# Kernel optimization log

Hardware: AMD Instinct MI355X
Metric: run time of the kernel (lower is better)

Reference implementation:

```python
import jax, jax.numpy as jnp
import numpy as np

B, S, D, H = 2, 2048, 1024, 16
HD = D // H  # head_dim = 64


def setup_inputs() -> dict:
    key = jax.random.key(0)
    ks = jax.random.split(key, 5)
    scale = 1.0 / np.sqrt(D)
    return {
        "x": jax.random.normal(ks[0], (B, S, D), dtype=jnp.float32),
        "w_qkv": jax.random.normal(ks[1], (D, 3 * D), dtype=jnp.float32) * scale,
        "b_qkv": jnp.zeros((3 * D,), dtype=jnp.float32),
        "w_out": jax.random.normal(ks[2], (D, D), dtype=jnp.float32) * scale,
        "b_out": jnp.zeros((D,), dtype=jnp.float32),
    }


def reference(x, w_qkv, b_qkv, w_out, b_out):
    b, s, d = x.shape
    qkv = x @ w_qkv + b_qkv  # [B,S,3D]
    q, k, v = jnp.split(qkv, 3, axis=-1)
    # [B,S,D] -> [B,H,S,HD]
    def to_heads(t):
        return t.reshape(b, s, H, HD).transpose(0, 2, 1, 3)
    q, k, v = to_heads(q), to_heads(k), to_heads(v)
    scores = jnp.einsum("bhqd,bhkd->bhqk", q, k) / np.sqrt(HD)
    attn = jax.nn.softmax(scores, axis=-1)
    out = jnp.einsum("bhqk,bhkd->bhqd", attn, v)  # [B,H,S,HD]
    out = out.transpose(0, 2, 1, 3).reshape(b, s, d)
    return out @ w_out + b_out
```

## Files before the change

### kernel.cpp

```cpp
#include <hip/hip_runtime.h>
#include <hip/hip_bf16.h>
#include <math.h>


typedef __bf16 bf16;
typedef __attribute__((ext_vector_type(8))) __bf16 bf16x8;
typedef __attribute__((ext_vector_type(4))) __bf16 bf16x4;
typedef __attribute__((ext_vector_type(4))) float f32x4;

#define B_ 2
#define S_ 2048
#define D_ 1024
#define H_ 16
#define HD_ 64

__device__ __forceinline__ f32x4 mfma16(bf16x8 a, bf16x8 b, f32x4 c) {
    return __builtin_amdgcn_mfma_f32_16x16x32_bf16(a, b, c, 0, 0, 0);
}

__device__ __forceinline__ void gload_lds16(const void* g, void* l) {
    __builtin_amdgcn_global_load_lds(
        (const __attribute__((address_space(1))) void*)g,
        (__attribute__((address_space(3))) void*)l, 16, 0, 0);
}


__global__ __launch_bounds__(256) void convert_x_kernel(
        const float* __restrict__ x, bf16* __restrict__ xb) {
    int i = blockIdx.x * 256 + threadIdx.x;
    float4 v = ((const float4*)x)[i];
    bf16x4 o = { (bf16)v.x, (bf16)v.y, (bf16)v.z, (bf16)v.w };
    ((bf16x4*)xb)[i] = o;
}

__global__ __launch_bounds__(256) void transpose_w_kernel(
        const float* __restrict__ src, bf16* __restrict__ dst, int K, int N) {
    int n0 = blockIdx.x * 64, k0 = blockIdx.y * 64;
    int lane = threadIdx.x & 63, wv = threadIdx.x >> 6;
    int k = k0 + lane;
    for (int i = 0; i < 16; i++) {
        int n = n0 + wv * 16 + i;
        dst[(size_t)n * K + k] = (bf16)src[(size_t)k * N + n];
    }
}

template <bool OUT_BF16>
__global__ __launch_bounds__(256) void gemm_bt_kernel(
        const bf16* __restrict__ A, const bf16* __restrict__ Bt,
        const float* __restrict__ bias, void* __restrict__ Cout,
        int M, int N, int K) {
    __shared__ bf16 As[128 * 32];
    __shared__ bf16 Bs[128 * 32];
    const int t = threadIdx.x;
    const int lane = t & 63, w = t >> 6;
    const int g = lane >> 4, c = lane & 15;
    const int m0 = blockIdx.y * 128, n0 = blockIdx.x * 128;
    const int wm = (w >> 1) * 64, wn = (w & 1) * 64;

    f32x4 acc[4][4];
    for (int i = 0; i < 4; i++)
        for (int j = 0; j < 4; j++) acc[i][j] = (f32x4){0.f, 0.f, 0.f, 0.f};

    const size_t rowB = (size_t)K * 2;
    const char* Abase = (const char*)A + (size_t)m0 * rowB;
    const char* Bbase = (const char*)Bt + (size_t)n0 * rowB;

    for (int kt = 0; kt < K; kt += 32) {
        for (int i = 0; i < 2; i++) {
            int boff = (w * 2 + i) * 1024 + lane * 16;
            int row = boff >> 6;
            int colb = boff & 63;
            gload_lds16(Abase + (size_t)row * rowB + (size_t)kt * 2 + colb,
                        (char*)As + (w * 2 + i) * 1024);
            gload_lds16(Bbase + (size_t)row * rowB + (size_t)kt * 2 + colb,
                        (char*)Bs + (w * 2 + i) * 1024);
        }
        __syncthreads();
        bf16x8 af[4], bfr[4];
        for (int mt = 0; mt < 4; mt++)
            af[mt] = *(const bf16x8*)&As[(wm + mt * 16 + c) * 32 + g * 8];
        for (int nt = 0; nt < 4; nt++)
            bfr[nt] = *(const bf16x8*)&Bs[(wn + nt * 16 + c) * 32 + g * 8];
        for (int mt = 0; mt < 4; mt++)
            for (int nt = 0; nt < 4; nt++)
                acc[mt][nt] = mfma16(af[mt], bfr[nt], acc[mt][nt]);
        __syncthreads();
    }

    for (int mt = 0; mt < 4; mt++) {
        for (int nt = 0; nt < 4; nt++) {
            int col = n0 + wn + nt * 16 + c;
            float bv = bias[col];
            for (int r = 0; r < 4; r++) {
                int row = m0 + wm + mt * 16 + g * 4 + r;
                float v = acc[mt][nt][r] + bv;
                if (OUT_BF16)
                    ((bf16*)Cout)[(size_t)row * N + col] = (bf16)v;
                else
                    ((float*)Cout)[(size_t)row * N + col] = v;
            }
        }
    }
}

#define KT_ 64
#define LPK_ 72
#define LPP_ 76

__global__ __launch_bounds__(256) void attn_kernel(
        const bf16* __restrict__ qkv, bf16* __restrict__ out) {
    __shared__ bf16 Ks[2][KT_ * LPK_];
    __shared__ bf16 Vs[2][HD_ * LPK_];
    __shared__ bf16 Ps[4][2][16 * LPP_];

    const int t = threadIdx.x;
    const int lane = t & 63, wv = t >> 6;
    const int g = lane >> 4, c = lane & 15;
    const int bh = blockIdx.y, b = bh >> 4, h = bh & 15;
    const int qbase = blockIdx.x * 128 + wv * 16;

    const float cs = 0.125f * 1.44269504088896341f;

    bf16x8 qf[2][2];
    for (int ch = 0; ch < 2; ch++) {
        const size_t qoff = (size_t)(b * S_ + qbase + ch * 64 + c) * (3 * D_) + h * HD_;
        qf[ch][0] = *(const bf16x8*)(qkv + qoff + g * 8);
        qf[ch][1] = *(const bf16x8*)(qkv + qoff + 32 + g * 8);
    }

    const bf16 one = (bf16)1.0f;
    const bf16x8 ones = { one, one, one, one, one, one, one, one };

    f32x4 o[2][4];
    for (int ch = 0; ch < 2; ch++)
        for (int i = 0; i < 4; i++) o[ch][i] = (f32x4){0.f, 0.f, 0.f, 0.f};
    f32x4 accl[2];
    accl[0] = accl[1] = (f32x4){0.f, 0.f, 0.f, 0.f};

    const int kk = t >> 2, kh = (t & 3) * 16;
    const int vk = t & 63, vh = (t >> 6) * 16;

    const bf16* kbase = qkv + (size_t)(b * S_) * (3 * D_) + D_ + h * HD_;
    const bf16* vbase = qkv + (size_t)(b * S_) * (3 * D_) + 2 * D_ + h * HD_;

    bf16x8 kr0, kr1, vr0, vr1;
    {
        const bf16* ks = kbase + (size_t)kk * (3 * D_) + kh;
        kr0 = *(const bf16x8*)ks;
        kr1 = *(const bf16x8*)(ks + 8);
        const bf16* vs = vbase + (size_t)vk * (3 * D_) + vh;
        vr0 = *(const bf16x8*)vs;
        vr1 = *(const bf16x8*)(vs + 8);
        *(bf16x8*)&Ks[0][kk * LPK_ + kh] = kr0;
        *(bf16x8*)&Ks[0][kk * LPK_ + kh + 8] = kr1;
        for (int j = 0; j < 8; j++) Vs[0][(vh + j) * LPK_ + vk] = vr0[j];
        for (int j = 0; j < 8; j++) Vs[0][(vh + 8 + j) * LPK_ + vk] = vr1[j];
    }
    __syncthreads();

    for (int tile = 0; tile < S_ / KT_; tile++) {
        const int buf = tile & 1;
        const bool has_next = (tile + 1) < (S_ / KT_);
        if (has_next) {
            const int j0 = (tile + 1) * KT_;
            const bf16* ks = kbase + (size_t)(j0 + kk) * (3 * D_) + kh;
            kr0 = *(const bf16x8*)ks;
            kr1 = *(const bf16x8*)(ks + 8);
            const bf16* vs = vbase + (size_t)(j0 + vk) * (3 * D_) + vh;
            vr0 = *(const bf16x8*)vs;
            vr1 = *(const bf16x8*)(vs + 8);
        }

        bf16x8 kf0[4], kf1[4];
        for (int kt = 0; kt < 4; kt++) {
            kf0[kt] = *(const bf16x8*)&Ks[buf][(kt * 16 + c) * LPK_ + g * 8];
            kf1[kt] = *(const bf16x8*)&Ks[buf][(kt * 16 + c) * LPK_ + 32 + g * 8];
        }

        f32x4 s[2][4];
        for (int ch = 0; ch < 2; ch++)
            for (int kt = 0; kt < 4; kt++) {
                f32x4 acc = (f32x4){0.f, 0.f, 0.f, 0.f};
                acc = mfma16(qf[ch][0], kf0[kt], acc);
                acc = mfma16(qf[ch][1], kf1[kt], acc);
                s[ch][kt] = acc;
            }

        for (int ch = 0; ch < 2; ch++) {
            bf16* P = Ps[wv][ch];
            for (int kt = 0; kt < 4; kt++)
                for (int r = 0; r < 4; r++)
                    P[(g * 4 + r) * LPP_ + kt * 16 + c] =
                        (bf16)__builtin_amdgcn_exp2f(s[ch][kt][r] * cs);
        }

        bf16x8 pf[2][2];
        for (int ch = 0; ch < 2; ch++) {
            pf[ch][0] = *(const bf16x8*)&Ps[wv][ch][c * LPP_ + g * 8];
            pf[ch][1] = *(const bf16x8*)&Ps[wv][ch][c * LPP_ + 32 + g * 8];
            accl[ch] = mfma16(pf[ch][0], ones, accl[ch]);
            accl[ch] = mfma16(pf[ch][1], ones, accl[ch]);
        }

        for (int nt = 0; nt < 4; nt++) {
            bf16x8 vf0 = *(const bf16x8*)&Vs[buf][(nt * 16 + c) * LPK_ + g * 8];
            bf16x8 vf1 = *(const bf16x8*)&Vs[buf][(nt * 16 + c) * LPK_ + 32 + g * 8];
            for (int ch = 0; ch < 2; ch++) {
                o[ch][nt] = mfma16(pf[ch][0], vf0, o[ch][nt]);
                o[ch][nt] = mfma16(pf[ch][1], vf1, o[ch][nt]);
            }
        }

        if (has_next) {
            *(bf16x8*)&Ks[buf ^ 1][kk * LPK_ + kh] = kr0;
            *(bf16x8*)&Ks[buf ^ 1][kk * LPK_ + kh + 8] = kr1;
            for (int j = 0; j < 8; j++) Vs[buf ^ 1][(vh + j) * LPK_ + vk] = vr0[j];
            for (int j = 0; j < 8; j++) Vs[buf ^ 1][(vh + 8 + j) * LPK_ + vk] = vr1[j];
        }
        __syncthreads();
    }

    for (int ch = 0; ch < 2; ch++)
        for (int r = 0; r < 4; r++) {
            float inv = 1.f / accl[ch][r];
            int row = qbase + ch * 64 + g * 4 + r;
            size_t base = (size_t)(b * S_ + row) * D_ + h * HD_;
            for (int nt = 0; nt < 4; nt++)
                out[base + nt * 16 + c] = (bf16)(o[ch][nt][r] * inv);
        }
}


extern "C" void kernel_launch(void* const* d_in, const int* in_sizes, int n_in,
                              void* d_out, int out_size, void* d_ws, size_t ws_size,
                              hipStream_t stream) {
    const float* x     = (const float*)d_in[0];
    const float* w_qkv = (const float*)d_in[1];
    const float* b_qkv = (const float*)d_in[2];
    const float* w_out = (const float*)d_in[3];
    const float* b_out = (const float*)d_in[4];
    float* out = (float*)d_out;

    char* ws = (char*)d_ws;
    bf16* x_bf    = (bf16*)(ws + 0);
    bf16* attn_bf = x_bf;
    bf16* wqkv_t  = (bf16*)(ws + (8u << 20));
    bf16* wout_t  = (bf16*)(ws + (14u << 20));
    bf16* qkv_bf  = (bf16*)(ws + (16u << 20));

    convert_x_kernel<<<(B_ * S_ * D_) / (256 * 4), 256, 0, stream>>>(x, x_bf);
    transpose_w_kernel<<<dim3(3 * D_ / 64, D_ / 64), 256, 0, stream>>>(w_qkv, wqkv_t, D_, 3 * D_);
    transpose_w_kernel<<<dim3(D_ / 64, D_ / 64), 256, 0, stream>>>(w_out, wout_t, D_, D_);

    gemm_bt_kernel<true><<<dim3(3 * D_ / 128, B_ * S_ / 128), 256, 0, stream>>>(
        x_bf, wqkv_t, b_qkv, qkv_bf, B_ * S_, 3 * D_, D_);

    attn_kernel<<<dim3(S_ / 128, B_ * H_), 256, 0, stream>>>(qkv_bf, attn_bf);

    gemm_bt_kernel<false><<<dim3(D_ / 128, B_ * S_ / 128), 256, 0, stream>>>(
        attn_bf, wout_t, b_out, out, B_ * S_, D_, D_);
}
```

Baseline: 226.4 us.

## Keep attention probabilities in registers via transposed MFMA and permuted K rows

The attention kernel now computes S^T = K·Q^T with a permuted K row layout in shared memory, so the exp'd scores land in registers already shaped as the B operand for the P·V MFMA. This removes the per-wave LDS round-trip for P and the extra ones-MFMA for row sums, which are now register adds plus a two-step cross-lane shuffle. The output store becomes vectorized bf16x4. Separately, the weight transpose kernel is rewritten to stage through padded shared memory so both global reads and writes are coalesced and vectorized.

```diff
diff --git a/kernel.cpp b/kernel.cpp
--- a/kernel.cpp
+++ b/kernel.cpp
@@ -35,12 +35,25 @@
 
 __global__ __launch_bounds__(256) void transpose_w_kernel(
         const float* __restrict__ src, bf16* __restrict__ dst, int K, int N) {
-    int n0 = blockIdx.x * 64, k0 = blockIdx.y * 64;
-    int lane = threadIdx.x & 63, wv = threadIdx.x >> 6;
-    int k = k0 + lane;
-    for (int i = 0; i < 16; i++) {
-        int n = n0 + wv * 16 + i;
-        dst[(size_t)n * K + k] = (bf16)src[(size_t)k * N + n];
+    __shared__ bf16 Ls[64 * 65];
+    const int t = threadIdx.x;
+    const int n0 = blockIdx.x * 64, k0 = blockIdx.y * 64;
+    for (int p = 0; p < 4; p++) {
+        int r = p * 16 + (t >> 4);
+        int c4 = (t & 15) * 4;
+        float4 v = *(const float4*)&src[(size_t)(k0 + r) * N + n0 + c4];
+        Ls[r * 65 + c4 + 0] = (bf16)v.x;
+        Ls[r * 65 + c4 + 1] = (bf16)v.y;
+        Ls[r * 65 + c4 + 2] = (bf16)v.z;
+        Ls[r * 65 + c4 + 3] = (bf16)v.w;
+    }
+    __syncthreads();
+    for (int p = 0; p < 4; p++) {
+        int nl = p * 16 + (t >> 4);
+        int kc = (t & 15) * 4;
+        bf16x4 o = { Ls[(kc + 0) * 65 + nl], Ls[(kc + 1) * 65 + nl],
+                     Ls[(kc + 2) * 65 + nl], Ls[(kc + 3) * 65 + nl] };
+        *(bf16x4*)&dst[(size_t)(n0 + nl) * K + k0 + kc] = o;
     }
 }
 
@@ -105,13 +118,11 @@
 
 #define KT_ 64
 #define LPK_ 72
-#define LPP_ 76
 
 __global__ __launch_bounds__(256) void attn_kernel(
         const bf16* __restrict__ qkv, bf16* __restrict__ out) {
     __shared__ bf16 Ks[2][KT_ * LPK_];
     __shared__ bf16 Vs[2][HD_ * LPK_];
-    __shared__ bf16 Ps[4][2][16 * LPP_];
 
     const int t = threadIdx.x;
     const int lane = t & 63, wv = t >> 6;
@@ -128,16 +139,15 @@
         qf[ch][1] = *(const bf16x8*)(qkv + qoff + 32 + g * 8);
     }
 
-    const bf16 one = (bf16)1.0f;
-    const bf16x8 ones = { one, one, one, one, one, one, one, one };
-
     f32x4 o[2][4];
     for (int ch = 0; ch < 2; ch++)
         for (int i = 0; i < 4; i++) o[ch][i] = (f32x4){0.f, 0.f, 0.f, 0.f};
-    f32x4 accl[2];
-    accl[0] = accl[1] = (f32x4){0.f, 0.f, 0.f, 0.f};
+    f32x4 lsum[2];
+    lsum[0] = lsum[1] = (f32x4){0.f, 0.f, 0.f, 0.f};
 
     const int kk = t >> 2, kh = (t & 3) * 16;
+    const int krow = ((kk >> 5) & 1) * 32 + ((kk >> 2) & 1) * 16 +
+                     ((kk >> 3) & 3) * 4 + (kk & 3);
     const int vk = t & 63, vh = (t >> 6) * 16;
 
     const bf16* kbase = qkv + (size_t)(b * S_) * (3 * D_) + D_ + h * HD_;
@@ -151,8 +161,8 @@
         const bf16* vs = vbase + (size_t)vk * (3 * D_) + vh;
         vr0 = *(const bf16x8*)vs;
         vr1 = *(const bf16x8*)(vs + 8);
-        *(bf16x8*)&Ks[0][kk * LPK_ + kh] = kr0;
-        *(bf16x8*)&Ks[0][kk * LPK_ + kh + 8] = kr1;
+        *(bf16x8*)&Ks[0][krow * LPK_ + kh] = kr0;
+        *(bf16x8*)&Ks[0][krow * LPK_ + kh + 8] = kr1;
         for (int j = 0; j < 8; j++) Vs[0][(vh + j) * LPK_ + vk] = vr0[j];
         for (int j = 0; j < 8; j++) Vs[0][(vh + 8 + j) * LPK_ + vk] = vr1[j];
     }
@@ -177,57 +187,55 @@
             kf1[kt] = *(const bf16x8*)&Ks[buf][(kt * 16 + c) * LPK_ + 32 + g * 8];
         }
 
-        f32x4 s[2][4];
-        for (int ch = 0; ch < 2; ch++)
+        for (int ch = 0; ch < 2; ch++) {
+            f32x4 p[4];
             for (int kt = 0; kt < 4; kt++) {
                 f32x4 acc = (f32x4){0.f, 0.f, 0.f, 0.f};
-                acc = mfma16(qf[ch][0], kf0[kt], acc);
-                acc = mfma16(qf[ch][1], kf1[kt], acc);
-                s[ch][kt] = acc;
-            }
-
-        for (int ch = 0; ch < 2; ch++) {
-            bf16* P = Ps[wv][ch];
-            for (int kt = 0; kt < 4; kt++)
+                acc = mfma16(kf0[kt], qf[ch][0], acc);
+                acc = mfma16(kf1[kt], qf[ch][1], acc);
                 for (int r = 0; r < 4; r++)
-                    P[(g * 4 + r) * LPP_ + kt * 16 + c] =
-                        (bf16)__builtin_amdgcn_exp2f(s[ch][kt][r] * cs);
-        }
-
-        bf16x8 pf[2][2];
-        for (int ch = 0; ch < 2; ch++) {
-            pf[ch][0] = *(const bf16x8*)&Ps[wv][ch][c * LPP_ + g * 8];
-            pf[ch][1] = *(const bf16x8*)&Ps[wv][ch][c * LPP_ + 32 + g * 8];
-            accl[ch] = mfma16(pf[ch][0], ones, accl[ch]);
-            accl[ch] = mfma16(pf[ch][1], ones, accl[ch]);
-        }
-
-        for (int nt = 0; nt < 4; nt++) {
-            bf16x8 vf0 = *(const bf16x8*)&Vs[buf][(nt * 16 + c) * LPK_ + g * 8];
-            bf16x8 vf1 = *(const bf16x8*)&Vs[buf][(nt * 16 + c) * LPK_ + 32 + g * 8];
-            for (int ch = 0; ch < 2; ch++) {
-                o[ch][nt] = mfma16(pf[ch][0], vf0, o[ch][nt]);
-                o[ch][nt] = mfma16(pf[ch][1], vf1, o[ch][nt]);
+                    p[kt][r] = __builtin_amdgcn_exp2f(acc[r] * cs);
+            }
+            lsum[ch] += (p[0] + p[1]) + (p[2] + p[3]);
+
+            bf16x8 pb0, pb1;
+            for (int r = 0; r < 4; r++) {
+                pb0[r]     = (bf16)p[0][r];
+                pb0[4 + r] = (bf16)p[1][r];
+                pb1[r]     = (bf16)p[2][r];
+                pb1[4 + r] = (bf16)p[3][r];
+            }
+
+            for (int nt = 0; nt < 4; nt++) {
+                bf16x8 vf0 = *(const bf16x8*)&Vs[buf][(nt * 16 + c) * LPK_ + g * 8];
+                bf16x8 vf1 = *(const bf16x8*)&Vs[buf][(nt * 16 + c) * LPK_ + 32 + g * 8];
+                o[ch][nt] = mfma16(vf0, pb0, o[ch][nt]);
+                o[ch][nt] = mfma16(vf1, pb1, o[ch][nt]);
             }
         }
 
         if (has_next) {
-            *(bf16x8*)&Ks[buf ^ 1][kk * LPK_ + kh] = kr0;
-            *(bf16x8*)&Ks[buf ^ 1][kk * LPK_ + kh + 8] = kr1;
+            *(bf16x8*)&Ks[buf ^ 1][krow * LPK_ + kh] = kr0;
+            *(bf16x8*)&Ks[buf ^ 1][krow * LPK_ + kh + 8] = kr1;
             for (int j = 0; j < 8; j++) Vs[buf ^ 1][(vh + j) * LPK_ + vk] = vr0[j];
             for (int j = 0; j < 8; j++) Vs[buf ^ 1][(vh + 8 + j) * LPK_ + vk] = vr1[j];
         }
         __syncthreads();
     }
 
-    for (int ch = 0; ch < 2; ch++)
-        for (int r = 0; r < 4; r++) {
-            float inv = 1.f / accl[ch][r];
-            int row = qbase + ch * 64 + g * 4 + r;
-            size_t base = (size_t)(b * S_ + row) * D_ + h * HD_;
-            for (int nt = 0; nt < 4; nt++)
-                out[base + nt * 16 + c] = (bf16)(o[ch][nt][r] * inv);
-        }
+    for (int ch = 0; ch < 2; ch++) {
+        float lh = (lsum[ch][0] + lsum[ch][1]) + (lsum[ch][2] + lsum[ch][3]);
+        lh += __shfl_xor(lh, 16);
+        lh += __shfl_xor(lh, 32);
+        float inv = 1.f / lh;
+        int q = qbase + ch * 64 + c;
+        size_t base = (size_t)(b * S_ + q) * D_ + h * HD_ + g * 4;
+        for (int nt = 0; nt < 4; nt++) {
+            bf16x4 ov = { (bf16)(o[ch][nt][0] * inv), (bf16)(o[ch][nt][1] * inv),
+                          (bf16)(o[ch][nt][2] * inv), (bf16)(o[ch][nt][3] * inv) };
+            *(bf16x4*)&out[base + nt * 16] = ov;
+        }
+    }
 }
 
 
```

Result: faster. 203.2 us (-10.2%).
